# Kernel optimization log

Measured on AMD Instinct MI355X. Metric: run time of the kernel, lower is better.

The kernel has to match this reference:

```python
import jax, jax.numpy as jnp
import numpy as np
import math

B, L, IN_F, OUT_F = 16, 4096, 384, 384
SCALE = 1.0 / math.sqrt(IN_F)
EPS = 1e-8


def setup_inputs() -> dict:
    key = jax.random.key(0)
    k1, k2, k3 = jax.random.split(key, 3)
    return {
        "Efou": jax.random.normal(k1, (B, L, IN_F), dtype=jnp.float32),
        "y": jax.random.normal(k2, (B, IN_F), dtype=jnp.float32),
        "weight": jax.random.normal(k3, (1, OUT_F, IN_F), dtype=jnp.float32),
    }


def reference(Efou, y, weight):
    b, size_patch, in_f = Efou.shape
    out_f = weight.shape[1]
    # per-sample weight modulation: [B, out, in]
    w = SCALE * weight * y[:, None, :]
    # demodulation
    dconf = jax.lax.rsqrt(jnp.sum(w * w, axis=2) + EPS)  # [B, out]
    w = w * dconf[:, :, None]
    # Faithful raw reshape of [B, L, in] buffer to [B, in, L] layout (NOT a transpose),
    # matching torch's Efou.reshape(1, B*in, L) + grouped conv1d with kernel size 1.
    Xr = Efou.reshape(b, in_f, size_patch)
    out = jnp.einsum("boi,bip->bop", w, Xr)  # [B, out, L]
    # Faithful raw view of (B*out, L) buffer as (B, L, out)
    return out.reshape(b, size_patch, out_f)
```

## Files before the change

### kernel.cpp

```cpp
#include <hip/hip_runtime.h>
#include <hip/hip_bf16.h>
#include <stdint.h>

#define Bn 16
#define Ln 4096
#define KF 384
#define OF 384

#define BM 128
#define BN 128
#define BK 64
#define LDX 72

static constexpr float kScale = 0.051031036307982884f;

typedef __attribute__((ext_vector_type(4))) float f32x4;
typedef __attribute__((ext_vector_type(2))) float f32x2;
typedef __attribute__((ext_vector_type(8))) short short8;
typedef __attribute__((ext_vector_type(4))) float floatx4;
typedef __attribute__((ext_vector_type(4))) unsigned int uint4v;

__device__ __forceinline__ void gl_lds16(const void* g, void* l) {
  __builtin_amdgcn_global_load_lds(
      (const __attribute__((address_space(1))) unsigned int*)g,
      (__attribute__((address_space(3))) unsigned int*)l, 16, 0, 0);
}

__device__ __forceinline__ unsigned int f2bf_bits(float f) {
  union { float f; unsigned int u; } v;
  v.f = f;
  return (v.u + 0x7FFFu + ((v.u >> 16) & 1u)) >> 16;
}
__device__ __forceinline__ unsigned int pack2bf(float lo, float hi) {
  return f2bf_bits(lo) | (f2bf_bits(hi) << 16);
}

__global__ __launch_bounds__(256) void modw_kernel(const float* __restrict__ weight,
                                                   const float* __restrict__ y,
                                                   unsigned short* __restrict__ wmod) {
  int t = threadIdx.x;
  int wv = t >> 6, lane = t & 63;
  int row = blockIdx.x * 4 + wv;
  int b = row / OF, o = row % OF;
  const float* wr = weight + o * KF;
  const float* yr = y + b * KF;
  float vals[6];
  float ss = 0.f;
#pragma unroll
  for (int j = 0; j < 3; ++j) {
    int k = (lane + 64 * j) * 2;
    f32x2 wvv = *(const f32x2*)(wr + k);
    f32x2 yv = *(const f32x2*)(yr + k);
    float t0 = kScale * wvv[0] * yv[0];
    float t1 = kScale * wvv[1] * yv[1];
    vals[2 * j] = t0;
    vals[2 * j + 1] = t1;
    ss += t0 * t0 + t1 * t1;
  }
#pragma unroll
  for (int off = 32; off >= 1; off >>= 1) ss += __shfl_xor(ss, off, 64);
  float d = rsqrtf(ss + 1e-8f);
  unsigned short* orow = wmod + row * KF;
#pragma unroll
  for (int j = 0; j < 3; ++j) {
    int k = (lane + 64 * j) * 2;
    *(unsigned int*)(orow + k) = pack2bf(vals[2 * j] * d, vals[2 * j + 1] * d);
  }
}

__global__ __launch_bounds__(256) void gemm_kernel(const float* __restrict__ X,
                                                   const unsigned short* __restrict__ Wm,
                                                   float* __restrict__ out) {
  __shared__ unsigned short sA[BM * BK];
  __shared__ unsigned short sX[BN * LDX];

  int flat = blockIdx.x;
  int logical = (flat & 7) * 192 + (flat >> 3);
  int mt = logical % 3;
  int nt = (logical / 3) & 31;
  int b = logical / 96;

  int t = threadIdx.x;
  int wave = t >> 6, lane = t & 63;
  int quad = lane >> 4;

  const float* Xb = X + b * (KF * Ln);
  const unsigned short* Wb = Wm + (b * OF + mt * BM) * KF;
  int pbase = nt * BN;

  floatx4 acc[4][4] = {};

  int p0 = (t & 31) * 4;
  int kr0 = (t >> 5) * 8;
  int arow = (wave >> 1) * 64 + (lane & 15);
  int brow = (wave & 1) * 64 + (lane & 15);

  for (int kc = 0; kc < 6; ++kc) {
    int k0 = kc * BK;
#pragma unroll
    for (int j = 0; j < 4; ++j) {
      int boff = wave * 4096 + j * 1024 + lane * 16;
      int row = boff >> 7;
      int kb = (boff & 127) >> 1;
      gl_lds16(Wb + row * KF + k0 + kb, (char*)sA + boff);
    }
    const float* xsrc = Xb + (k0 + kr0) * Ln + pbase + p0;
    f32x4 xv[8];
#pragma unroll
    for (int i = 0; i < 8; ++i) xv[i] = *(const f32x4*)(xsrc + i * Ln);
#pragma unroll
    for (int j = 0; j < 4; ++j) {
      uint4v wvec;
#pragma unroll
      for (int i = 0; i < 4; ++i)
        wvec[i] = pack2bf(xv[2 * i][j], xv[2 * i + 1][j]);
      *(uint4v*)(&sX[(p0 + j) * LDX + kr0]) = wvec;
    }
    __syncthreads();
#pragma unroll
    for (int s = 0; s < 2; ++s) {
      int kk = s * 32 + quad * 8;
      short8 af[4], bf[4];
#pragma unroll
      for (int mi = 0; mi < 4; ++mi)
        af[mi] = *(const short8*)(&sA[(arow + mi * 16) * BK + kk]);
#pragma unroll
      for (int ni = 0; ni < 4; ++ni)
        bf[ni] = *(const short8*)(&sX[(brow + ni * 16) * LDX + kk]);
#pragma unroll
      for (int mi = 0; mi < 4; ++mi)
#pragma unroll
        for (int ni = 0; ni < 4; ++ni)
          acc[mi][ni] = __builtin_amdgcn_mfma_f32_16x16x32_bf16(af[mi], bf[ni], acc[mi][ni], 0, 0, 0);
    }
    __syncthreads();
  }

  float* outb = out + (b * OF + mt * BM) * Ln + pbase;
  int col = lane & 15;
#pragma unroll
  for (int mi = 0; mi < 4; ++mi) {
    int ob = (wave >> 1) * 64 + mi * 16 + quad * 4;
#pragma unroll
    for (int ni = 0; ni < 4; ++ni) {
      int p = (wave & 1) * 64 + ni * 16 + col;
#pragma unroll
      for (int r = 0; r < 4; ++r) outb[(ob + r) * Ln + p] = acc[mi][ni][r];
    }
  }
}

extern "C" void kernel_launch(void* const* d_in, const int* in_sizes, int n_in,
                              void* d_out, int out_size, void* d_ws, size_t ws_size,
                              hipStream_t stream) {
  const float* Efou = (const float*)d_in[0];
  const float* y = (const float*)d_in[1];
  const float* weight = (const float*)d_in[2];
  float* out = (float*)d_out;
  unsigned short* wmod = (unsigned short*)d_ws;

  modw_kernel<<<(Bn * OF) / 4, 256, 0, stream>>>(weight, y, wmod);
  gemm_kernel<<<Bn * (OF / BM) * (Ln / BN), 256, 0, stream>>>(Efou, wmod, out);
}
```

Before: 205.0 us.

## Double-buffer weight tiles, prefetch next X chunk, and XOR-swizzle LDS layouts

New measurement: 203.5 us. About the same (-0.7%).

```diff
diff --git a/kernel.cpp b/kernel.cpp
--- a/kernel.cpp
+++ b/kernel.cpp
@@ -68,10 +68,10 @@
   }
 }
 
-__global__ __launch_bounds__(256) void gemm_kernel(const float* __restrict__ X,
-                                                   const unsigned short* __restrict__ Wm,
-                                                   float* __restrict__ out) {
-  __shared__ unsigned short sA[BM * BK];
+__global__ __launch_bounds__(256, 3) void gemm_kernel(const float* __restrict__ X,
+                                                      const unsigned short* __restrict__ Wm,
+                                                      float* __restrict__ out) {
+  __shared__ unsigned short sA[2][BM * BK];
   __shared__ unsigned short sX[BN * LDX];
 
   int flat = blockIdx.x;
@@ -90,50 +90,90 @@
 
   floatx4 acc[4][4] = {};
 
-  int p0 = (t & 31) * 4;
+  int i31 = t & 31;
+  int p0 = i31 * 4;
   int kr0 = (t >> 5) * 8;
+  int kr0s = (((t >> 5) ^ (i31 & 7)) * 8);
   int arow = (wave >> 1) * 64 + (lane & 15);
   int brow = (wave & 1) * 64 + (lane & 15);
-
+  int asw = lane & 7;
+  int xsw = ((lane & 15) >> 2);
+
+  int aoff[4], asrc_row[4], asrc_c[4];
+#pragma unroll
+  for (int j = 0; j < 4; ++j) {
+    int boff = wave * 4096 + j * 1024 + lane * 16;
+    int row = boff >> 7;
+    int cp = (boff >> 4) & 7;
+    aoff[j] = boff;
+    asrc_row[j] = row;
+    asrc_c[j] = (cp ^ (row & 7)) * 8;
+  }
+
+  f32x4 xv[8];
+  unsigned int wv4[4][4];
+
+#pragma unroll
+  for (int j = 0; j < 4; ++j)
+    gl_lds16(Wb + asrc_row[j] * KF + 0 + asrc_c[j], (char*)sA[0] + aoff[j]);
+  {
+    const float* xsrc = Xb + (0 + kr0) * Ln + pbase + p0;
+#pragma unroll
+    for (int i = 0; i < 8; ++i) xv[i] = *(const f32x4*)(xsrc + i * Ln);
+#pragma unroll
+    for (int j = 0; j < 4; ++j)
+#pragma unroll
+      for (int i = 0; i < 4; ++i)
+        wv4[j][i] = pack2bf(xv[2 * i][j], xv[2 * i + 1][j]);
+#pragma unroll
+    for (int j = 0; j < 4; ++j)
+      *(uint4v*)(&sX[(p0 + j) * LDX + kr0s]) = *(uint4v*)wv4[j];
+  }
+  __syncthreads();
+
+#pragma unroll
   for (int kc = 0; kc < 6; ++kc) {
-    int k0 = kc * BK;
-#pragma unroll
-    for (int j = 0; j < 4; ++j) {
-      int boff = wave * 4096 + j * 1024 + lane * 16;
-      int row = boff >> 7;
-      int kb = (boff & 127) >> 1;
-      gl_lds16(Wb + row * KF + k0 + kb, (char*)sA + boff);
-    }
-    const float* xsrc = Xb + (k0 + kr0) * Ln + pbase + p0;
-    f32x4 xv[8];
-#pragma unroll
-    for (int i = 0; i < 8; ++i) xv[i] = *(const f32x4*)(xsrc + i * Ln);
-#pragma unroll
-    for (int j = 0; j < 4; ++j) {
-      uint4v wvec;
-#pragma unroll
-      for (int i = 0; i < 4; ++i)
-        wvec[i] = pack2bf(xv[2 * i][j], xv[2 * i + 1][j]);
-      *(uint4v*)(&sX[(p0 + j) * LDX + kr0]) = wvec;
-    }
-    __syncthreads();
+    int cur = kc & 1;
+    if (kc < 5) {
+      int k0n = (kc + 1) * BK;
+#pragma unroll
+      for (int j = 0; j < 4; ++j)
+        gl_lds16(Wb + asrc_row[j] * KF + k0n + asrc_c[j], (char*)sA[cur ^ 1] + aoff[j]);
+      const float* xsrc = Xb + (k0n + kr0) * Ln + pbase + p0;
+#pragma unroll
+      for (int i = 0; i < 8; ++i) xv[i] = *(const f32x4*)(xsrc + i * Ln);
+    }
 #pragma unroll
     for (int s = 0; s < 2; ++s) {
-      int kk = s * 32 + quad * 8;
       short8 af[4], bf[4];
 #pragma unroll
-      for (int mi = 0; mi < 4; ++mi)
-        af[mi] = *(const short8*)(&sA[(arow + mi * 16) * BK + kk]);
-#pragma unroll
-      for (int ni = 0; ni < 4; ++ni)
-        bf[ni] = *(const short8*)(&sX[(brow + ni * 16) * LDX + kk]);
+      for (int mi = 0; mi < 4; ++mi) {
+        int ca = (((s << 2) | quad) ^ asw) * 8;
+        af[mi] = *(const short8*)(&sA[cur][(arow + mi * 16) * BK + ca]);
+      }
+#pragma unroll
+      for (int ni = 0; ni < 4; ++ni) {
+        int cx = (((s << 2) | quad) ^ (((ni & 1) << 2) | xsw)) * 8;
+        bf[ni] = *(const short8*)(&sX[(brow + ni * 16) * LDX + cx]);
+      }
 #pragma unroll
       for (int mi = 0; mi < 4; ++mi)
 #pragma unroll
         for (int ni = 0; ni < 4; ++ni)
           acc[mi][ni] = __builtin_amdgcn_mfma_f32_16x16x32_bf16(af[mi], bf[ni], acc[mi][ni], 0, 0, 0);
     }
-    __syncthreads();
+    if (kc < 5) {
+#pragma unroll
+      for (int j = 0; j < 4; ++j)
+#pragma unroll
+        for (int i = 0; i < 4; ++i)
+          wv4[j][i] = pack2bf(xv[2 * i][j], xv[2 * i + 1][j]);
+      __syncthreads();
+#pragma unroll
+      for (int j = 0; j < 4; ++j)
+        *(uint4v*)(&sX[(p0 + j) * LDX + kr0s]) = *(uint4v*)wv4[j];
+      __syncthreads();
+    }
   }
 
   float* outb = out + (b * OF + mt * BM) * Ln + pbase;
```

## Pre-transpose input to bf16 and double-buffer GEMM with async LDS loads

Applied to the files above, without the earlier changes.

Result: slower. 213.0 us (+3.9%).

```diff
diff --git a/kernel.cpp b/kernel.cpp
--- a/kernel.cpp
+++ b/kernel.cpp
@@ -9,8 +9,7 @@
 
 #define BM 128
 #define BN 128
-#define BK 64
-#define LDX 72
+#define BK 32
 
 static constexpr float kScale = 0.051031036307982884f;
 
@@ -19,6 +18,7 @@
 typedef __attribute__((ext_vector_type(8))) short short8;
 typedef __attribute__((ext_vector_type(4))) float floatx4;
 typedef __attribute__((ext_vector_type(4))) unsigned int uint4v;
+typedef __attribute__((ext_vector_type(2))) unsigned int uint2v;
 
 __device__ __forceinline__ void gl_lds16(const void* g, void* l) {
   __builtin_amdgcn_global_load_lds(
@@ -68,11 +68,44 @@
   }
 }
 
-__global__ __launch_bounds__(256) void gemm_kernel(const float* __restrict__ X,
-                                                   const unsigned short* __restrict__ Wm,
-                                                   float* __restrict__ out) {
-  __shared__ unsigned short sA[BM * BK];
-  __shared__ unsigned short sX[BN * LDX];
+__global__ __launch_bounds__(256) void tconv_kernel(const float* __restrict__ X,
+                                                    unsigned short* __restrict__ Xt) {
+  __shared__ unsigned short sT[64 * 72];
+  int bid = blockIdx.x;
+  int b = bid / 384;
+  int rem = bid % 384;
+  int kt = rem >> 6;
+  int pt = rem & 63;
+  const float* src = X + b * (KF * Ln) + (kt * 64) * Ln + pt * 64;
+  int t = threadIdx.x;
+  int p0 = (t & 15) * 4;
+  int kr0 = (t >> 4) * 4;
+  f32x4 xv[4];
+#pragma unroll
+  for (int i = 0; i < 4; ++i) xv[i] = *(const f32x4*)(src + (kr0 + i) * Ln + p0);
+#pragma unroll
+  for (int j = 0; j < 4; ++j) {
+    uint2v v;
+    v[0] = pack2bf(xv[0][j], xv[1][j]);
+    v[1] = pack2bf(xv[2][j], xv[3][j]);
+    *(uint2v*)(&sT[(p0 + j) * 72 + kr0]) = v;
+  }
+  __syncthreads();
+  unsigned short* dst = Xt + b * (Ln * KF) + (pt * 64) * KF + kt * 64;
+#pragma unroll
+  for (int s = 0; s < 2; ++s) {
+    int slot = t + 256 * s;
+    int p = slot >> 3, kseg = slot & 7;
+    uint4v v = *(const uint4v*)(&sT[p * 72 + kseg * 8]);
+    *(uint4v*)(dst + p * KF + kseg * 8) = v;
+  }
+}
+
+__global__ __launch_bounds__(256, 4) void gemm_kernel(const unsigned short* __restrict__ Xt,
+                                                      const unsigned short* __restrict__ Wm,
+                                                      float* __restrict__ out) {
+  __shared__ unsigned short sA[2][BM * BK];
+  __shared__ unsigned short sX[2][BN * BK];
 
   int flat = blockIdx.x;
   int logical = (flat & 7) * 192 + (flat >> 3);
@@ -84,59 +117,57 @@
   int wave = t >> 6, lane = t & 63;
   int quad = lane >> 4;
 
-  const float* Xb = X + b * (KF * Ln);
   const unsigned short* Wb = Wm + (b * OF + mt * BM) * KF;
-  int pbase = nt * BN;
+  const unsigned short* Xb = Xt + b * (Ln * KF) + (nt * BN) * KF;
 
   floatx4 acc[4][4] = {};
 
-  int p0 = (t & 31) * 4;
-  int kr0 = (t >> 5) * 8;
+  int so[2], srow[2], sks[2];
+#pragma unroll
+  for (int j = 0; j < 2; ++j) {
+    int boff = (wave * 2 + j) * 1024 + lane * 16;
+    so[j] = boff;
+    srow[j] = boff >> 6;
+    sks[j] = (boff & 63) >> 1;
+  }
+
   int arow = (wave >> 1) * 64 + (lane & 15);
   int brow = (wave & 1) * 64 + (lane & 15);
+  int kq = quad * 8;
 
-  for (int kc = 0; kc < 6; ++kc) {
-    int k0 = kc * BK;
 #pragma unroll
-    for (int j = 0; j < 4; ++j) {
-      int boff = wave * 4096 + j * 1024 + lane * 16;
-      int row = boff >> 7;
-      int kb = (boff & 127) >> 1;
-      gl_lds16(Wb + row * KF + k0 + kb, (char*)sA + boff);
+  for (int j = 0; j < 2; ++j) {
+    gl_lds16(Wb + srow[j] * KF + sks[j], (char*)sA[0] + so[j]);
+    gl_lds16(Xb + srow[j] * KF + sks[j], (char*)sX[0] + so[j]);
+  }
+  __syncthreads();
+
+  for (int kc = 0; kc < 12; ++kc) {
+    int cur = kc & 1;
+    if (kc < 11) {
+      int k0 = (kc + 1) * BK;
+#pragma unroll
+      for (int j = 0; j < 2; ++j) {
+        gl_lds16(Wb + srow[j] * KF + k0 + sks[j], (char*)sA[cur ^ 1] + so[j]);
+        gl_lds16(Xb + srow[j] * KF + k0 + sks[j], (char*)sX[cur ^ 1] + so[j]);
+      }
     }
-    const float* xsrc = Xb + (k0 + kr0) * Ln + pbase + p0;
-    f32x4 xv[8];
+    short8 af[4], bf[4];
 #pragma unroll
-    for (int i = 0; i < 8; ++i) xv[i] = *(const f32x4*)(xsrc + i * Ln);
+    for (int mi = 0; mi < 4; ++mi)
+      af[mi] = *(const short8*)(&sA[cur][(arow + mi * 16) * BK + kq]);
 #pragma unroll
-    for (int j = 0; j < 4; ++j) {
-      uint4v wvec;
+    for (int ni = 0; ni < 4; ++ni)
+      bf[ni] = *(const short8*)(&sX[cur][(brow + ni * 16) * BK + kq]);
 #pragma unroll
-      for (int i = 0; i < 4; ++i)
-        wvec[i] = pack2bf(xv[2 * i][j], xv[2 * i + 1][j]);
-      *(uint4v*)(&sX[(p0 + j) * LDX + kr0]) = wvec;
-    }
-    __syncthreads();
-#pragma unroll
-    for (int s = 0; s < 2; ++s) {
-      int kk = s * 32 + quad * 8;
-      short8 af[4], bf[4];
-#pragma unroll
-      for (int mi = 0; mi < 4; ++mi)
-        af[mi] = *(const short8*)(&sA[(arow + mi * 16) * BK + kk]);
+    for (int mi = 0; mi < 4; ++mi)
 #pragma unroll
       for (int ni = 0; ni < 4; ++ni)
-        bf[ni] = *(const short8*)(&sX[(brow + ni * 16) * LDX + kk]);
-#pragma unroll
-      for (int mi = 0; mi < 4; ++mi)
-#pragma unroll
-        for (int ni = 0; ni < 4; ++ni)
-          acc[mi][ni] = __builtin_amdgcn_mfma_f32_16x16x32_bf16(af[mi], bf[ni], acc[mi][ni], 0, 0, 0);
-    }
+        acc[mi][ni] = __builtin_amdgcn_mfma_f32_16x16x32_bf16(af[mi], bf[ni], acc[mi][ni], 0, 0, 0);
     __syncthreads();
   }
 
-  float* outb = out + (b * OF + mt * BM) * Ln + pbase;
+  float* outb = out + (b * OF + mt * BM) * Ln + nt * BN;
   int col = lane & 15;
 #pragma unroll
   for (int mi = 0; mi < 4; ++mi) {
@@ -158,7 +189,9 @@
   const float* weight = (const float*)d_in[2];
   float* out = (float*)d_out;
   unsigned short* wmod = (unsigned short*)d_ws;
+  unsigned short* Xtr = (unsigned short*)((char*)d_ws + (8u << 20));
 
   modw_kernel<<<(Bn * OF) / 4, 256, 0, stream>>>(weight, y, wmod);
-  gemm_kernel<<<Bn * (OF / BM) * (Ln / BN), 256, 0, stream>>>(Efou, wmod, out);
+  tconv_kernel<<<Bn * (KF / 64) * (Ln / 64), 256, 0, stream>>>(Efou, Xtr);
+  gemm_kernel<<<Bn * (OF / BM) * (Ln / BN), 256, 0, stream>>>(Xtr, wmod, out);
 }
```
